# Kernel optimization log

Hardware: AMD Instinct MI355X
Metric: run time of the kernel (lower is better)

Reference implementation:

```python
import jax, jax.numpy as jnp
import numpy as np

N_HEAD = 8


def setup_inputs() -> dict:
    key = jax.random.key(0)
    ks = jax.random.split(key, 5)
    D = 512
    q = jax.random.normal(ks[0], (2, 4096, D), dtype=jnp.float32)
    s = 0.02  # init scale for weights
    Wq = jax.random.normal(ks[1], (D, D), dtype=jnp.float32) * s
    Wk = jax.random.normal(ks[2], (D, D), dtype=jnp.float32) * s
    Wv = jax.random.normal(ks[3], (D, D), dtype=jnp.float32) * s
    Wo = jax.random.normal(ks[4], (D, D), dtype=jnp.float32) * s
    z = jnp.zeros((D,), dtype=jnp.float32)
    return {"q": q, "Wq": Wq, "bq": z, "Wk": Wk, "bk": z, "Wv": Wv, "bv": z, "Wo": Wo, "bo": z}


def _split_heads(x, n_head):
    # (b, s, c) -> (b, h, s, c//h)
    b, s, c = x.shape
    return x.reshape(b, s, n_head, c // n_head).transpose(0, 2, 1, 3)


def reference(q, Wq, bq, Wk, bk, Wv, bv, Wo, bo):
    # Linear projections (nn.Linear: x @ W.T + b); self-attention (kv = q)
    qp = _split_heads(q @ Wq.T + bq, N_HEAD)  # (b, h, s, dh)
    kp = _split_heads(q @ Wk.T + bk, N_HEAD)
    vp = _split_heads(q @ Wv.T + bv, N_HEAD)
    dh = qp.shape[-1]
    scale = 1.0 / jnp.sqrt(jnp.asarray(dh, dtype=qp.dtype))
    # unfused MATH-backend SDPA: full [b,h,s,s] scores, stable softmax, no dropout (eval)
    scores = jnp.einsum("bhqd,bhkd->bhqk", qp, kp) * scale
    probs = jax.nn.softmax(scores, axis=-1)
    attn = jnp.einsum("bhqk,bhkd->bhqd", probs, vp)  # (b, h, s, dh)
    # merge heads: (b, h, s, dh) -> (b, s, h*dh)
    b, h, s, _ = attn.shape
    merged = attn.transpose(0, 2, 1, 3).reshape(b, s, h * dh)
    return merged @ Wo.T + bo
```

## Files before the change

kernel.cpp:

```cpp
#include <hip/hip_runtime.h>
#include <hip/hip_bf16.h>
#include <math.h>

typedef __attribute__((ext_vector_type(8))) short bf16x8;
typedef __attribute__((ext_vector_type(4))) short bf16x4;
typedef __attribute__((ext_vector_type(4))) float f32x4;

__device__ __forceinline__ unsigned short f2bf(float f) {
    union { float f; unsigned int u; } v; v.f = f;
    unsigned int u = v.u;
    u += 0x7fffu + ((u >> 16) & 1u);
    return (unsigned short)(u >> 16);
}

__device__ __forceinline__ f32x4 mfma16(bf16x4 a, bf16x4 b, f32x4 c) {
#if __has_builtin(__builtin_amdgcn_mfma_f32_16x16x16bf16_1k)
    return __builtin_amdgcn_mfma_f32_16x16x16bf16_1k(a, b, c, 0, 0, 0);
#else
    asm volatile("v_mfma_f32_16x16x16_bf16 %0, %1, %2, %0\n\ts_nop 7"
                 : "+v"(c) : "v"(a), "v"(b));
    return c;
#endif
}

__device__ __forceinline__ unsigned packbf2(float a, float b) {
    __hip_bfloat162 h = __float22bfloat162_rn(float2{a, b});
    union { __hip_bfloat162 h; unsigned u; } v; v.h = h;
    return v.u;
}

__device__ __forceinline__ float fmax3(float a, float b, float c) {
    return fmaxf(fmaxf(a, b), c);
}

template<int A_BF16>
__device__ __forceinline__ void gemm_body(const void* Ap, const float* W,
                                          f32x4 (&acc)[4][4],
                                          unsigned short (*As)[40], unsigned short (*Bs)[40],
                                          int bm, int bn, int t)
{
    constexpr int Kdim = 512;
    const int lane = t & 63, g = lane >> 4, c = lane & 15;
    const int w = t >> 6, wr = w >> 1, wc = w & 1;

    uint4  paB[2];
    float4 paF[4];
    float4 pw[4];
    const int ccB = (t & 3) * 8, r0B = t >> 2;
    const int c4  = (t & 7) * 4, r0F = t >> 3;

    if (A_BF16) {
        const unsigned short* A = (const unsigned short*)Ap;
        for (int p = 0; p < 2; ++p)
            paB[p] = *(const uint4*)(A + (size_t)(bm + r0B + p * 64) * Kdim + ccB);
    } else {
        const float* A = (const float*)Ap;
        for (int p = 0; p < 4; ++p)
            paF[p] = *(const float4*)(A + (size_t)(bm + r0F + p * 32) * Kdim + c4);
    }
    for (int p = 0; p < 4; ++p)
        pw[p] = *(const float4*)(W + (size_t)(bn + r0F + p * 32) * Kdim + c4);

    for (int k0 = 0; k0 < Kdim; k0 += 32) {
        __syncthreads();
        if (A_BF16) {
            for (int p = 0; p < 2; ++p)
                *(uint4*)&As[r0B + p * 64][ccB] = paB[p];
        } else {
            for (int p = 0; p < 4; ++p) {
                float4 v = paF[p];
                ushort4 hv;
                hv.x = f2bf(v.x); hv.y = f2bf(v.y); hv.z = f2bf(v.z); hv.w = f2bf(v.w);
                *(ushort4*)&As[r0F + p * 32][c4] = hv;
            }
        }
        for (int p = 0; p < 4; ++p) {
            float4 v = pw[p];
            ushort4 hv;
            hv.x = f2bf(v.x); hv.y = f2bf(v.y); hv.z = f2bf(v.z); hv.w = f2bf(v.w);
            *(ushort4*)&Bs[r0F + p * 32][c4] = hv;
        }
        __syncthreads();
        if (k0 + 32 < Kdim) {
            const int kn = k0 + 32;
            if (A_BF16) {
                const unsigned short* A = (const unsigned short*)Ap;
                for (int p = 0; p < 2; ++p)
                    paB[p] = *(const uint4*)(A + (size_t)(bm + r0B + p * 64) * Kdim + kn + ccB);
            } else {
                const float* A = (const float*)Ap;
                for (int p = 0; p < 4; ++p)
                    paF[p] = *(const float4*)(A + (size_t)(bm + r0F + p * 32) * Kdim + kn + c4);
            }
            for (int p = 0; p < 4; ++p)
                pw[p] = *(const float4*)(W + (size_t)(bn + r0F + p * 32) * Kdim + kn + c4);
        }
        bf16x8 af[4], bfr[4];
        for (int i = 0; i < 4; ++i)
            af[i] = *(const bf16x8*)&As[wr * 64 + i * 16 + c][g * 8];
        for (int j = 0; j < 4; ++j)
            bfr[j] = *(const bf16x8*)&Bs[wc * 64 + j * 16 + c][g * 8];
        for (int i = 0; i < 4; ++i)
            for (int j = 0; j < 4; ++j)
                acc[i][j] = __builtin_amdgcn_mfma_f32_16x16x32_bf16(af[i], bfr[j], acc[i][j], 0, 0, 0);
    }
}

__global__ __launch_bounds__(256, 2)
void gemm_qkv(const float* __restrict__ q,
              const float* __restrict__ Wq, const float* __restrict__ bq,
              const float* __restrict__ Wk, const float* __restrict__ bk,
              const float* __restrict__ Wv, const float* __restrict__ bv,
              unsigned short* __restrict__ Qo, unsigned short* __restrict__ Ko,
              unsigned short* __restrict__ Vo)
{
    __shared__ unsigned short As[128][40];
    __shared__ unsigned short Bs[128][40];
    const int t = threadIdx.x, z = blockIdx.z;
    const int lane = t & 63, g = lane >> 4, c = lane & 15;
    const int w = t >> 6, wr = w >> 1, wc = w & 1;
    const int bm = blockIdx.x * 128, bn = blockIdx.y * 128;

    const float* W    = (z == 0) ? Wq : (z == 1) ? Wk : Wv;
    const float* bias = (z == 0) ? bq : (z == 1) ? bk : bv;
    unsigned short* Out = (z == 0) ? Qo : (z == 1) ? Ko : Vo;

    f32x4 acc[4][4] = {};
    gemm_body<0>((const void*)q, W, acc, As, Bs, bm, bn, t);

    float bv4[4];
    for (int j = 0; j < 4; ++j) bv4[j] = bias[bn + wc * 64 + j * 16 + c];
    for (int i = 0; i < 4; ++i)
        for (int j = 0; j < 4; ++j)
            for (int r = 0; r < 4; ++r) {
                int m = bm + wr * 64 + i * 16 + 4 * g + r;
                int n = bn + wc * 64 + j * 16 + c;
                float val = acc[i][j][r] + bv4[j];
                int b = m >> 12, s = m & 4095, h = n >> 6, d = n & 63;
                if (z < 2)
                    Out[((((size_t)b * 8 + h) * 4096 + s) << 6) + d] = f2bf(val);
                else
                    Out[(((size_t)b * 8 + h) * 64 + d) * 4096 + s] = f2bf(val);
            }
}

__global__ __launch_bounds__(256, 2)
void gemm_out(const unsigned short* __restrict__ A, const float* __restrict__ W,
              const float* __restrict__ bias, float* __restrict__ Out)
{
    __shared__ unsigned short As[128][40];
    __shared__ unsigned short Bs[128][40];
    const int t = threadIdx.x;
    const int lane = t & 63, g = lane >> 4, c = lane & 15;
    const int w = t >> 6, wr = w >> 1, wc = w & 1;
    const int bm = blockIdx.x * 128, bn = blockIdx.y * 128;

    f32x4 acc[4][4] = {};
    gemm_body<1>((const void*)A, W, acc, As, Bs, bm, bn, t);

    float bv4[4];
    for (int j = 0; j < 4; ++j) bv4[j] = bias[bn + wc * 64 + j * 16 + c];
    for (int i = 0; i < 4; ++i)
        for (int j = 0; j < 4; ++j)
            for (int r = 0; r < 4; ++r) {
                int m = bm + wr * 64 + i * 16 + 4 * g + r;
                int n = bn + wc * 64 + j * 16 + c;
                Out[(size_t)m * 512 + n] = acc[i][j][r] + bv4[j];
            }
}

__global__ __launch_bounds__(256, 2)
void attn64(const unsigned short* __restrict__ Q, const unsigned short* __restrict__ Kh,
            const unsigned short* __restrict__ VT, unsigned short* __restrict__ Mo)
{
    __shared__ unsigned short Ks[64][72];
    __shared__ unsigned short Vs[64][72];

    const int t = threadIdx.x, w = t >> 6, lane = t & 63, g = lane >> 4, c = lane & 15;
    const int idp = (blockIdx.x & 7) * 128 + (blockIdx.x >> 3);
    const int bh = idp >> 6;
    const int q0 = (idp & 63) * 64;
    const unsigned short* Qb = Q + (size_t)bh * 4096 * 64;
    const unsigned short* Kb = Kh + (size_t)bh * 4096 * 64;
    const unsigned short* Vb = VT + (size_t)bh * 64 * 4096;

    bf16x8 qf[2];
    {
        int qr = q0 + w * 16 + c;
        qf[0] = *(const bf16x8*)(Qb + (size_t)qr * 64 + g * 8);
        qf[1] = *(const bf16x8*)(Qb + (size_t)qr * 64 + 32 + g * 8);
    }

    f32x4 o[4] = {};
    f32x4 lacc = {};
    float nm2 = 0.f;

    bf16x4 ones;
    ones[0] = ones[1] = ones[2] = ones[3] = (short)0x3F80;

    const int srow = t >> 2, scol = (t & 3) * 16;
    const unsigned short* kp0 = Kb + (size_t)srow * 64 + scol;
    const unsigned short* vp0 = Vb + (size_t)srow * 4096 + scol;

    uint4 ka0 = *(const uint4*)(kp0);
    uint4 ka1 = *(const uint4*)(kp0 + 8);
    uint4 va0 = *(const uint4*)(vp0);
    uint4 va1 = *(const uint4*)(vp0 + 8);

    const float sc2 = 0.125f * 1.44269504f;
    const float THR = 10.f;

    for (int jt = 0; jt < 64; ++jt) {
        __syncthreads();
        *(uint4*)&Ks[srow][scol]     = ka0;
        *(uint4*)&Ks[srow][scol + 8] = ka1;
        *(uint4*)&Vs[srow][scol]     = va0;
        *(uint4*)&Vs[srow][scol + 8] = va1;
        __syncthreads();
        if (jt < 63) {
            const unsigned short* kp = kp0 + (size_t)(jt + 1) * 4096;
            ka0 = *(const uint4*)(kp);
            ka1 = *(const uint4*)(kp + 8);
            const unsigned short* vp = vp0 + (jt + 1) * 64;
            va0 = *(const uint4*)(vp);
            va1 = *(const uint4*)(vp + 8);
        }

        f32x4 t4[4];
        for (int nt = 0; nt < 4; ++nt) {
            bf16x8 kf0 = *(const bf16x8*)&Ks[nt * 16 + c][g * 8];
            bf16x8 kf1 = *(const bf16x8*)&Ks[nt * 16 + c][32 + g * 8];
            f32x4 z = {};
            z = __builtin_amdgcn_mfma_f32_16x16x32_bf16(kf0, qf[0], z, 0, 0, 0);
            z = __builtin_amdgcn_mfma_f32_16x16x32_bf16(kf1, qf[1], z, 0, 0, 0);
            for (int r = 0; r < 4; ++r) t4[nt][r] = fmaf(z[r], sc2, nm2);
        }

        float ma = fmax3(t4[0][0], t4[0][1], t4[0][2]);
        float mb = fmax3(t4[0][3], t4[1][0], t4[1][1]);
        float mc = fmax3(t4[1][2], t4[1][3], t4[2][0]);
        float md = fmax3(t4[2][1], t4[2][2], t4[2][3]);
        float me = fmax3(t4[3][0], t4[3][1], t4[3][2]);
        float tm = fmax3(fmax3(ma, mb, mc), fmax3(md, me, t4[3][3]), -3.0e38f);
        if (!__all(tm <= THR)) {
            float pm = tm;
            pm = fmaxf(pm, __shfl_xor(pm, 16));
            pm = fmaxf(pm, __shfl_xor(pm, 32));
            float dm = fmaxf(pm, 0.f);
            nm2 -= dm;
            float alpha = exp2f(-dm);
            for (int nt = 0; nt < 4; ++nt)
                for (int r = 0; r < 4; ++r) t4[nt][r] -= dm;
            for (int r = 0; r < 4; ++r) {
                float ar = __shfl(alpha, 4 * g + r);
                for (int nd = 0; nd < 4; ++nd) o[nd][r] *= ar;
                lacc[r] *= ar;
            }
        }

        bf16x4 pf[4];
        for (int nt = 0; nt < 4; ++nt) {
            float p0 = exp2f(t4[nt][0]), p1 = exp2f(t4[nt][1]);
            float p2 = exp2f(t4[nt][2]), p3 = exp2f(t4[nt][3]);
            union { unsigned u[2]; bf16x4 v; } pk;
            pk.u[0] = packbf2(p0, p1);
            pk.u[1] = packbf2(p2, p3);
            pf[nt] = pk.v;
        }

        for (int nd = 0; nd < 4; ++nd)
            for (int nt = 0; nt < 4; ++nt) {
                bf16x4 vf = *(const bf16x4*)&Vs[nd * 16 + c][nt * 16 + 4 * g];
                o[nd] = mfma16(pf[nt], vf, o[nd]);
            }
        for (int nt = 0; nt < 4; ++nt)
            lacc = mfma16(pf[nt], ones, lacc);
    }

    const int b = bh >> 3, h = bh & 7;
    for (int r = 0; r < 4; ++r) {
        float inv = 1.f / lacc[r];
        int m = b * 4096 + q0 + w * 16 + 4 * g + r;
        for (int nd = 0; nd < 4; ++nd) {
            int n = h * 64 + nd * 16 + c;
            Mo[(size_t)m * 512 + n] = f2bf(o[nd][r] * inv);
        }
    }
}

extern "C" void kernel_launch(void* const* d_in, const int* in_sizes, int n_in,
                              void* d_out, int out_size, void* d_ws, size_t ws_size,
                              hipStream_t stream) {
    const float* q  = (const float*)d_in[0];
    const float* Wq = (const float*)d_in[1];
    const float* bq = (const float*)d_in[2];
    const float* Wk = (const float*)d_in[3];
    const float* bk = (const float*)d_in[4];
    const float* Wv = (const float*)d_in[5];
    const float* bv = (const float*)d_in[6];
    const float* Wo = (const float*)d_in[7];
    const float* bo = (const float*)d_in[8];

    unsigned short* Qb = (unsigned short*)d_ws;
    unsigned short* Kb = Qb + (size_t)16 * 4096 * 64;
    unsigned short* Vt = Kb + (size_t)16 * 4096 * 64;
    unsigned short* Mg = Vt + (size_t)16 * 4096 * 64;

    dim3 gb(256);
    dim3 gqkv(64, 4, 3);
    gemm_qkv<<<gqkv, gb, 0, stream>>>(q, Wq, bq, Wk, bk, Wv, bv, Qb, Kb, Vt);

    dim3 ga(1024);
    attn64<<<ga, gb, 0, stream>>>(Qb, Kb, Vt, Mg);

    dim3 gg(64, 4);
    gemm_out<<<gg, gb, 0, stream>>>(Mg, Wo, bo, (float*)d_out);
}
```

Before: 200.7 us.

## Double KV tile to 128 keys with XOR-swizzled LDS and MFMA priority hints

The attention kernel now stages 128 keys per iteration instead of 64, which halves the number of barrier pairs and global-load rounds. It processes each tile as two 64-key halves. Padded LDS rows are replaced by an XOR swizzle to avoid bank conflicts, and s_setprio raises wave priority around the MFMA sections. LDS use per block doubles, to 32KB from about 18KB, which could limit occupancy. More prefetch registers are also held live across the loop.

```diff
diff --git a/kernel.cpp b/kernel.cpp
--- a/kernel.cpp
+++ b/kernel.cpp
@@ -173,8 +173,8 @@
 void attn64(const unsigned short* __restrict__ Q, const unsigned short* __restrict__ Kh,
             const unsigned short* __restrict__ VT, unsigned short* __restrict__ Mo)
 {
-    __shared__ unsigned short Ks[64][72];
-    __shared__ unsigned short Vs[64][72];
+    __shared__ unsigned short Ks[128 * 64];
+    __shared__ unsigned short Vs[64 * 128];
 
     const int t = threadIdx.x, w = t >> 6, lane = t & 63, g = lane >> 4, c = lane & 15;
     const int idp = (blockIdx.x & 7) * 128 + (blockIdx.x >> 3);
@@ -198,83 +198,101 @@
     bf16x4 ones;
     ones[0] = ones[1] = ones[2] = ones[3] = (short)0x3F80;
 
-    const int srow = t >> 2, scol = (t & 3) * 16;
-    const unsigned short* kp0 = Kb + (size_t)srow * 64 + scol;
-    const unsigned short* vp0 = Vb + (size_t)srow * 4096 + scol;
-
-    uint4 ka0 = *(const uint4*)(kp0);
-    uint4 ka1 = *(const uint4*)(kp0 + 8);
-    uint4 va0 = *(const uint4*)(vp0);
-    uint4 va1 = *(const uint4*)(vp0 + 8);
+    const int krow = t >> 1, kcol = (t & 1) * 32;
+    const int vrow = t >> 2, vcol = (t & 3) * 32;
+    int kwoff[4], vwoff[4];
+    for (int b2 = 0; b2 < 4; ++b2) {
+        kwoff[b2] = krow * 64 + ((((kcol >> 3) + b2) ^ (krow & 7)) << 3);
+        vwoff[b2] = vrow * 128 + ((((vcol >> 3) + b2) ^ (vrow & 7)) << 3);
+    }
+    const unsigned short* kp0 = Kb + (size_t)krow * 64 + kcol;
+    const unsigned short* vp0 = Vb + (size_t)vrow * 4096 + vcol;
+
+    uint4 ka[4], va[4];
+    for (int b2 = 0; b2 < 4; ++b2) {
+        ka[b2] = *(const uint4*)(kp0 + b2 * 8);
+        va[b2] = *(const uint4*)(vp0 + b2 * 8);
+    }
 
     const float sc2 = 0.125f * 1.44269504f;
     const float THR = 10.f;
-
-    for (int jt = 0; jt < 64; ++jt) {
+    const int c7 = c & 7;
+
+    for (int jt = 0; jt < 32; ++jt) {
         __syncthreads();
-        *(uint4*)&Ks[srow][scol]     = ka0;
-        *(uint4*)&Ks[srow][scol + 8] = ka1;
-        *(uint4*)&Vs[srow][scol]     = va0;
-        *(uint4*)&Vs[srow][scol + 8] = va1;
+        for (int b2 = 0; b2 < 4; ++b2) {
+            *(uint4*)&Ks[kwoff[b2]] = ka[b2];
+            *(uint4*)&Vs[vwoff[b2]] = va[b2];
+        }
         __syncthreads();
-        if (jt < 63) {
-            const unsigned short* kp = kp0 + (size_t)(jt + 1) * 4096;
-            ka0 = *(const uint4*)(kp);
-            ka1 = *(const uint4*)(kp + 8);
-            const unsigned short* vp = vp0 + (jt + 1) * 64;
-            va0 = *(const uint4*)(vp);
-            va1 = *(const uint4*)(vp + 8);
-        }
-
-        f32x4 t4[4];
-        for (int nt = 0; nt < 4; ++nt) {
-            bf16x8 kf0 = *(const bf16x8*)&Ks[nt * 16 + c][g * 8];
-            bf16x8 kf1 = *(const bf16x8*)&Ks[nt * 16 + c][32 + g * 8];
-            f32x4 z = {};
-            z = __builtin_amdgcn_mfma_f32_16x16x32_bf16(kf0, qf[0], z, 0, 0, 0);
-            z = __builtin_amdgcn_mfma_f32_16x16x32_bf16(kf1, qf[1], z, 0, 0, 0);
-            for (int r = 0; r < 4; ++r) t4[nt][r] = fmaf(z[r], sc2, nm2);
-        }
-
-        float ma = fmax3(t4[0][0], t4[0][1], t4[0][2]);
-        float mb = fmax3(t4[0][3], t4[1][0], t4[1][1]);
-        float mc = fmax3(t4[1][2], t4[1][3], t4[2][0]);
-        float md = fmax3(t4[2][1], t4[2][2], t4[2][3]);
-        float me = fmax3(t4[3][0], t4[3][1], t4[3][2]);
-        float tm = fmax3(fmax3(ma, mb, mc), fmax3(md, me, t4[3][3]), -3.0e38f);
-        if (!__all(tm <= THR)) {
-            float pm = tm;
-            pm = fmaxf(pm, __shfl_xor(pm, 16));
-            pm = fmaxf(pm, __shfl_xor(pm, 32));
-            float dm = fmaxf(pm, 0.f);
-            nm2 -= dm;
-            float alpha = exp2f(-dm);
+        if (jt < 31) {
+            const unsigned short* kp = kp0 + (size_t)(jt + 1) * 128 * 64;
+            const unsigned short* vp = vp0 + (jt + 1) * 128;
+            for (int b2 = 0; b2 < 4; ++b2) {
+                ka[b2] = *(const uint4*)(kp + b2 * 8);
+                va[b2] = *(const uint4*)(vp + b2 * 8);
+            }
+        }
+
+        for (int half = 0; half < 2; ++half) {
+            f32x4 t4[4];
+            __builtin_amdgcn_s_setprio(1);
+            for (int nt = 0; nt < 4; ++nt) {
+                int row = (half * 4 + nt) * 16 + c;
+                bf16x8 kf0 = *(const bf16x8*)&Ks[row * 64 + ((g ^ c7) << 3)];
+                bf16x8 kf1 = *(const bf16x8*)&Ks[row * 64 + (((4 + g) ^ c7) << 3)];
+                f32x4 z = {};
+                z = __builtin_amdgcn_mfma_f32_16x16x32_bf16(kf0, qf[0], z, 0, 0, 0);
+                z = __builtin_amdgcn_mfma_f32_16x16x32_bf16(kf1, qf[1], z, 0, 0, 0);
+                for (int r = 0; r < 4; ++r) t4[nt][r] = fmaf(z[r], sc2, nm2);
+            }
+            __builtin_amdgcn_s_setprio(0);
+
+            float ma = fmax3(t4[0][0], t4[0][1], t4[0][2]);
+            float mb = fmax3(t4[0][3], t4[1][0], t4[1][1]);
+            float mc = fmax3(t4[1][2], t4[1][3], t4[2][0]);
+            float md = fmax3(t4[2][1], t4[2][2], t4[2][3]);
+            float me = fmax3(t4[3][0], t4[3][1], t4[3][2]);
+            float tm = fmax3(fmax3(ma, mb, mc), fmax3(md, me, t4[3][3]), -3.0e38f);
+            if (!__all(tm <= THR)) {
+                float pm = tm;
+                pm = fmaxf(pm, __shfl_xor(pm, 16));
+                pm = fmaxf(pm, __shfl_xor(pm, 32));
+                float dm = fmaxf(pm, 0.f);
+                nm2 -= dm;
+                float alpha = exp2f(-dm);
+                for (int nt = 0; nt < 4; ++nt)
+                    for (int r = 0; r < 4; ++r) t4[nt][r] -= dm;
+                for (int r = 0; r < 4; ++r) {
+                    float ar = __shfl(alpha, 4 * g + r);
+                    for (int nd = 0; nd < 4; ++nd) o[nd][r] *= ar;
+                    lacc[r] *= ar;
+                }
+            }
+
+            bf16x4 pf[4];
+            for (int nt = 0; nt < 4; ++nt) {
+                float p0 = exp2f(t4[nt][0]), p1 = exp2f(t4[nt][1]);
+                float p2 = exp2f(t4[nt][2]), p3 = exp2f(t4[nt][3]);
+                union { unsigned u[2]; bf16x4 v; } pk;
+                pk.u[0] = packbf2(p0, p1);
+                pk.u[1] = packbf2(p2, p3);
+                pf[nt] = pk.v;
+            }
+
+            __builtin_amdgcn_s_setprio(1);
+            for (int nd = 0; nd < 4; ++nd) {
+                int row = nd * 16 + c;
+                for (int nt = 0; nt < 4; ++nt) {
+                    int slot = (2 * (half * 4 + nt) + (g >> 1)) ^ c7;
+                    bf16x4 vf = *(const bf16x4*)&Vs[row * 128 + (slot << 3) + ((g & 1) << 2)];
+                    o[nd] = mfma16(pf[nt], vf, o[nd]);
+                }
+            }
             for (int nt = 0; nt < 4; ++nt)
-                for (int r = 0; r < 4; ++r) t4[nt][r] -= dm;
-            for (int r = 0; r < 4; ++r) {
-                float ar = __shfl(alpha, 4 * g + r);
-                for (int nd = 0; nd < 4; ++nd) o[nd][r] *= ar;
-                lacc[r] *= ar;
-            }
-        }
-
-        bf16x4 pf[4];
-        for (int nt = 0; nt < 4; ++nt) {
-            float p0 = exp2f(t4[nt][0]), p1 = exp2f(t4[nt][1]);
-            float p2 = exp2f(t4[nt][2]), p3 = exp2f(t4[nt][3]);
-            union { unsigned u[2]; bf16x4 v; } pk;
-            pk.u[0] = packbf2(p0, p1);
-            pk.u[1] = packbf2(p2, p3);
-            pf[nt] = pk.v;
-        }
-
-        for (int nd = 0; nd < 4; ++nd)
-            for (int nt = 0; nt < 4; ++nt) {
-                bf16x4 vf = *(const bf16x4*)&Vs[nd * 16 + c][nt * 16 + 4 * g];
-                o[nd] = mfma16(pf[nt], vf, o[nd]);
-            }
-        for (int nt = 0; nt < 4; ++nt)
-            lacc = mfma16(pf[nt], ones, lacc);
+                lacc = mfma16(pf[nt], ones, lacc);
+            __builtin_amdgcn_s_setprio(0);
+        }
     }
 
     const int b = bh >> 3, h = bh & 7;
```

Result: slower. 346.3 us (+72.6%).
